# Optimization experiments

Hardware: AMD Instinct MI355X
Metric: run time of the kernel (lower is better)

Reference implementation:

```python
import jax, jax.numpy as jnp
import numpy as np

N_DIM = 256
NHIDDEN = 256
NLAYERS = 4
LAMDA = 0.5
ALPHA = 0.1
MODAL_WEIGHT = 1.0
N_SPEAKERS = 2
B_DIA = 100   # number of dialogues
L_DIA = 40    # utterances per dialogue
N_UTT = B_DIA * L_DIA


def _cos_sim_blocks(x, B, L):
    # per-dialogue cosine-similarity blocks: x [N, d] -> [B, L, L]
    xb = x.reshape(B, L, -1)
    xn = xb / jnp.linalg.norm(xb, axis=-1, keepdims=True)
    cos = jnp.einsum('bid,bjd->bij', xn, xn) * 0.99999
    return 1.0 - jnp.arccos(cos) / jnp.pi


def setup_inputs() -> dict:
    key = jax.random.key(0)
    ks = jax.random.split(key, 8)
    return {
        'a': jax.random.normal(ks[0], (N_UTT, N_DIM), jnp.float32),
        'v': jax.random.normal(ks[1], (N_UTT, N_DIM), jnp.float32),
        'l': jax.random.normal(ks[2], (N_UTT, N_DIM), jnp.float32),
        'qmask': jax.random.uniform(ks[3], (L_DIA, B_DIA, N_SPEAKERS), jnp.float32),
        'spk_emb': jax.random.normal(ks[4], (N_SPEAKERS, N_DIM), jnp.float32) * 0.02,
        'W0': jax.random.normal(ks[5], (N_DIM, NHIDDEN), jnp.float32) / np.sqrt(N_DIM).astype(np.float32),
        'b0': jnp.zeros((NHIDDEN,), jnp.float32),
        'Wconvs': jax.random.normal(ks[6], (NLAYERS, NHIDDEN, NHIDDEN), jnp.float32) / np.sqrt(NHIDDEN).astype(np.float32),
        'dia_len_each': L_DIA,
        'n_dialogues': B_DIA,
    }


def reference(a, v, l, qmask, spk_emb, W0, b0, Wconvs, dia_len_each, n_dialogues):
    B, L = n_dialogues, dia_len_each
    N = B * L
    M = 3  # modals 'avl'

    # --- speaker embedding added to text modality (use_speaker) ---
    # torch.cat([qmask[:x, i, :] for i, x in enumerate(dia_len)]) with equal lengths
    q = jnp.transpose(qmask, (1, 0, 2)).reshape(N, -1)   # [N, n_speakers]
    spk_idx = jnp.argmax(q, axis=-1)                      # [N]
    l = l + spk_emb[spk_idx]

    feats = [a, v, l]
    normed = [f / jnp.linalg.norm(f, axis=-1, keepdims=True) for f in feats]

    # --- create_big_adj: block-diag per-modal cosine-sim blocks + cross-modal diagonals ---
    adj = jnp.zeros((M * N, M * N), jnp.float32)
    idx = jnp.arange(N).reshape(B, L)
    rows = idx[:, :, None]   # [B, L, 1]
    cols = idx[:, None, :]   # [B, 1, L]
    ar = jnp.arange(N)
    for m in range(M):
        sim = _cos_sim_blocks(feats[m], B, L)            # [B, L, L]
        adj = adj.at[m * N + rows, m * N + cols].set(sim)
    for m in range(M):
        for n in range(M):
            if m == n:
                continue
            cs = jnp.sum(normed[m] * normed[n], axis=-1) * 0.99999
            dia_sim = 1.0 - jnp.arccos(cs) / jnp.pi
            adj = adj.at[m * N + ar, n * N + ar].set(dia_sim * MODAL_WEIGHT)
    d = jnp.sum(adj, axis=1)
    dinv = d ** -0.5
    adj = adj * dinv[:, None] * dinv[None, :]            # D^-1/2 A D^-1/2

    # --- GCNII_lyc propagation (eval mode, variant=False, no dropout) ---
    x = jnp.concatenate(feats, axis=0)                   # [3N, n_dim]
    h0 = jax.nn.relu(x @ W0 + b0)
    h = h0
    for i in range(NLAYERS):
        theta = float(np.log(LAMDA / (i + 1) + 1.0))
        hi = adj @ h
        support = (1.0 - ALPHA) * hi + ALPHA * h0
        h = jax.nn.relu(theta * (support @ Wconvs[i]) + (1.0 - theta) * support)
    feat = jnp.concatenate([x, h], axis=-1)              # use_residue

    # regroup modalities per utterance: [N, 3*(n_dim+nhidden)]
    out = jnp.concatenate([feat[:N], feat[N:2 * N], feat[2 * N:3 * N]], axis=-1)
    return out
```

## Files before the change

kernel.cpp:

```cpp
#include <hip/hip_runtime.h>
#include <hip/hip_bf16.h>

#define N_UTT 4000
#define NDIM 256
#define B_DIA 100
#define L_DIA 40
#define NLAYERS 4

typedef __attribute__((ext_vector_type(8))) short short8;
typedef __attribute__((ext_vector_type(4))) float f32x4;

union bfpk4 { __hip_bfloat16 h[4]; uint2 u; };

__global__ void k_wt(const float* __restrict__ W0, const float* __restrict__ Wc,
                     __hip_bfloat16* __restrict__ Wt) {
  int k0 = blockIdx.x * 64, n0 = blockIdx.y * 64, g = blockIdx.z;
  int t = threadIdx.x;
  const float* src = (g == 0) ? W0 : (Wc + (g - 1) * NDIM * NDIM);
  __shared__ float tile[64][65];
  #pragma unroll
  for (int it = 0; it < 16; it++) {
    int e = t + 256 * it;
    int row = e >> 6, col = e & 63;
    tile[row][col] = src[(k0 + row) * NDIM + n0 + col];
  }
  __syncthreads();
  #pragma unroll
  for (int it = 0; it < 16; it++) {
    int e = t + 256 * it;
    int row = e >> 6, col = e & 63;
    Wt[(g * NDIM + n0 + row) * NDIM + k0 + col] = __float2bfloat16(tile[col][row]);
  }
}

__global__ __launch_bounds__(512, 1) void k_main(
    const float* __restrict__ a, const float* __restrict__ v,
    const float* __restrict__ lf, const float* __restrict__ qmask,
    const float* __restrict__ spk, const float* __restrict__ b0,
    const __hip_bfloat16* __restrict__ Wt, float* __restrict__ out) {
  __shared__ __hip_bfloat16 xls[3][L_DIA][264];
  __shared__ __hip_bfloat16 hls[3][NDIM][L_DIA];
  __shared__ __hip_bfloat16 sext[3][L_DIA][136];
  __shared__ float invn[120];
  __shared__ float dinv[120];
  __shared__ float psum[120][4];

  int b = blockIdx.x;
  int t = threadIdx.x;
  int w = t >> 6, ln = t & 63;
  int l15 = ln & 15, lk = (ln >> 4) * 8;
  const float inv_pi = 0.31830988618379067f;

  {
    unsigned int* sz = (unsigned int*)&sext[0][0][0];
    #pragma unroll
    for (int e = t; e < 3 * L_DIA * 136 / 2; e += 512) sz[e] = 0u;
  }
  for (int e = t; e < 120 * 64; e += 512) {
    int r = e >> 6, c4 = e & 63;
    int m = r / L_DIA, p = r - m * L_DIA;
    int i = b * L_DIA + p;
    float4 val;
    if (m == 0)      val = ((const float4*)a)[i * 64 + c4];
    else if (m == 1) val = ((const float4*)v)[i * 64 + c4];
    else {
      val = ((const float4*)lf)[i * 64 + c4];
      float q0 = qmask[(p * B_DIA + b) * 2 + 0];
      float q1 = qmask[(p * B_DIA + b) * 2 + 1];
      int s = (q1 > q0) ? 1 : 0;
      float4 sv = ((const float4*)spk)[s * 64 + c4];
      val.x += sv.x; val.y += sv.y; val.z += sv.z; val.w += sv.w;
    }
    ((float4*)out)[i * 384 + m * 128 + c4] = val;
    bfpk4 pk;
    pk.h[0] = __float2bfloat16(val.x); pk.h[1] = __float2bfloat16(val.y);
    pk.h[2] = __float2bfloat16(val.z); pk.h[3] = __float2bfloat16(val.w);
    *(uint2*)&xls[m][p][c4 * 4] = pk.u;
  }
  __syncthreads();

  if (t < 480) {
    int r = t >> 2, q4 = t & 3;
    int m = r / L_DIA, p = r - m * L_DIA;
    float s = 0.f;
    #pragma unroll
    for (int j = 0; j < 64; j++) {
      float xv = __bfloat162float(xls[m][p][q4 * 64 + j]);
      s += xv * xv;
    }
    psum[r][q4] = s;
  }
  __syncthreads();
  if (t < 120) invn[t] = rsqrtf(psum[t][0] + psum[t][1] + psum[t][2] + psum[t][3]);
  __syncthreads();

  #pragma unroll
  for (int it = 0; it < 5; it++) {
    int tau = w + 8 * it;
    if (tau < 36) {
      int mA, mB, rt, ct, isdiag = 0, slotA = 0, slotB = 0;
      if (tau < 27) {
        mA = tau / 9; int rc = tau - mA * 9; rt = rc / 3; ct = rc - rt * 3; mB = mA;
      } else {
        int pi = (tau - 27) / 3; rt = (tau - 27) - pi * 3; ct = rt;
        mA = (pi == 2) ? 1 : 0; mB = (pi == 0) ? 1 : 2;
        slotA = (pi == 0) ? 40 : 80; slotB = (pi == 2) ? 80 : 40;
        isdiag = 1;
      }
      int arow = rt * 16 + l15; if (arow > 39) arow = 39;
      int bcol = ct * 16 + l15; if (bcol > 39) bcol = 39;
      f32x4 acc = {0.f, 0.f, 0.f, 0.f};
      #pragma unroll
      for (int k0 = 0; k0 < NDIM; k0 += 32) {
        short8 af = *(const short8*)&xls[mA][arow][k0 + lk];
        short8 bf = *(const short8*)&xls[mB][bcol][k0 + lk];
        acc = __builtin_amdgcn_mfma_f32_16x16x32_bf16(af, bf, acc, 0, 0, 0);
      }
      #pragma unroll
      for (int rr = 0; rr < 4; rr++) {
        int row = rt * 16 + (ln >> 4) * 4 + rr;
        int col = ct * 16 + l15;
        if (!isdiag) {
          if (row < 40 && col < 40) {
            float cs = acc[rr] * invn[mA * 40 + row] * invn[mA * 40 + col] * 0.99999f;
            cs = fminf(fmaxf(cs, -1.f), 1.f);
            sext[mA][row][col] = __float2bfloat16(1.f - acosf(cs) * inv_pi);
          }
        } else {
          if (l15 == ((ln >> 4) * 4 + rr) && row < 40) {
            float cs = acc[rr] * invn[mA * 40 + row] * invn[mB * 40 + row] * 0.99999f;
            cs = fminf(fmaxf(cs, -1.f), 1.f);
            __hip_bfloat16 vv = __float2bfloat16(1.f - acosf(cs) * inv_pi);
            sext[mA][row][slotA + row] = vv;
            sext[mB][row][slotB + row] = vv;
          }
        }
      }
    }
  }
  __syncthreads();

  if (t < 120) {
    int m = t / 40, p = t - m * 40;
    float d = 0.f;
    #pragma unroll 10
    for (int q = 0; q < 40; q++) d += __bfloat162float(sext[m][p][q]);
    d += __bfloat162float(sext[m][p][40 + p]) + __bfloat162float(sext[m][p][80 + p]);
    dinv[t] = rsqrtf(d);
  }
  __syncthreads();
  for (int e = t; e < 5040; e += 512) {
    if (e < 4800) {
      int m = e / 1600, rem = e - m * 1600;
      int p = rem / 40, q = rem - p * 40;
      sext[m][p][q] = __float2bfloat16(
          __bfloat162float(sext[m][p][q]) * 0.9f * dinv[m * 40 + p] * dinv[m * 40 + q]);
    } else {
      int idx = e - 4800;
      int m = idx / 80, j = idx - m * 80;
      int which = j / 40, p = j - which * 40;
      int pmx = which ? ((m == 2) ? 1 : 2) : ((m == 0) ? 1 : 0);
      int k = 40 * (1 + which) + p;
      sext[m][p][k] = __float2bfloat16(
          __bfloat162float(sext[m][p][k]) * 0.9f * dinv[m * 40 + p] * dinv[pmx * 40 + p]);
    }
  }
  __syncthreads();

  uint2 h0r[9][2];
  #pragma unroll
  for (int s = 0; s < 9; s++) {
    int m = s / 3, rt = s - m * 3;
    int arow = rt * 16 + l15; if (arow > 39) arow = 39;
    int p0 = rt * 16 + (ln >> 4) * 4;
    #pragma unroll
    for (int c = 0; c < 2; c++) {
      int col = w * 32 + c * 16 + l15;
      f32x4 acc = {0.f, 0.f, 0.f, 0.f};
      #pragma unroll
      for (int k0 = 0; k0 < NDIM; k0 += 32) {
        short8 af = *(const short8*)&xls[m][arow][k0 + lk];
        short8 bf = *(const short8*)&Wt[col * NDIM + k0 + lk];
        acc = __builtin_amdgcn_mfma_f32_16x16x32_bf16(af, bf, acc, 0, 0, 0);
      }
      float bias = b0[col];
      bfpk4 pk;
      #pragma unroll
      for (int rr = 0; rr < 4; rr++)
        pk.h[rr] = __float2bfloat16(fmaxf(acc[rr] + bias, 0.f));
      h0r[s][c] = pk.u;
      if (p0 < 40) *(uint2*)&hls[m][col][p0] = pk.u;
    }
  }
  __syncthreads();

  const float thetas[NLAYERS] = {0.40546510810816438f, 0.22314355131420976f,
                                 0.15415067982725836f, 0.11778303565638346f};
  #pragma unroll
  for (int li = 0; li < NLAYERS; li++) {
    float th = thetas[li], onemt = 1.f - th;
    const __hip_bfloat16* Wl = Wt + (li + 1) * NDIM * NDIM;
    f32x4 supreg[9][2];
    #pragma unroll
    for (int s = 0; s < 9; s++) {
      int m = s / 3, rt = s - m * 3;
      int pm0 = (m == 0) ? 1 : 0;
      int pm1 = (m == 2) ? 1 : 2;
      int arow = rt * 16 + l15; if (arow > 39) arow = 39;
      int p0 = rt * 16 + (ln >> 4) * 4;
      #pragma unroll
      for (int c = 0; c < 2; c++) {
        int col = w * 32 + c * 16 + l15;
        f32x4 acc = {0.f, 0.f, 0.f, 0.f};
        #pragma unroll
        for (int j = 0; j < 4; j++) {
          int kk = j * 32 + lk;
          int srcm, brow;
          if (kk < 40)       { srcm = m;   brow = kk; }
          else if (kk < 80)  { srcm = pm0; brow = kk - 40; }
          else if (kk < 120) { srcm = pm1; brow = kk - 80; }
          else               { srcm = m;   brow = 0; }
          short8 af = *(const short8*)&sext[m][arow][j * 32 + lk];
          short8 bf = *(const short8*)&hls[srcm][col][brow];
          acc = __builtin_amdgcn_mfma_f32_16x16x32_bf16(af, bf, acc, 0, 0, 0);
        }
        bfpk4 h0p; h0p.u = h0r[s][c];
        #pragma unroll
        for (int rr = 0; rr < 4; rr++)
          acc[rr] += 0.1f * __bfloat162float(h0p.h[rr]);
        supreg[s][c] = acc;
        if (p0 < 40) {
          #pragma unroll
          for (int rr = 0; rr < 4; rr++)
            xls[m][p0 + rr][col] = __float2bfloat16(acc[rr]);
        }
      }
    }
    __syncthreads();
    #pragma unroll
    for (int s = 0; s < 9; s++) {
      int m = s / 3, rt = s - m * 3;
      int arow = rt * 16 + l15; if (arow > 39) arow = 39;
      int p0 = rt * 16 + (ln >> 4) * 4;
      #pragma unroll
      for (int c = 0; c < 2; c++) {
        int col = w * 32 + c * 16 + l15;
        f32x4 acc = {0.f, 0.f, 0.f, 0.f};
        #pragma unroll
        for (int k0 = 0; k0 < NDIM; k0 += 32) {
          short8 af = *(const short8*)&xls[m][arow][k0 + lk];
          short8 bf = *(const short8*)&Wl[col * NDIM + k0 + lk];
          acc = __builtin_amdgcn_mfma_f32_16x16x32_bf16(af, bf, acc, 0, 0, 0);
        }
        if (p0 < 40) {
          if (li < NLAYERS - 1) {
            bfpk4 pk;
            #pragma unroll
            for (int rr = 0; rr < 4; rr++)
              pk.h[rr] = __float2bfloat16(
                  fmaxf(th * acc[rr] + onemt * supreg[s][c][rr], 0.f));
            *(uint2*)&hls[m][col][p0] = pk.u;
          } else {
            #pragma unroll
            for (int rr = 0; rr < 4; rr++)
              out[(b * L_DIA + p0 + rr) * 1536 + m * 512 + 256 + col] =
                  fmaxf(th * acc[rr] + onemt * supreg[s][c][rr], 0.f);
          }
        }
      }
    }
    __syncthreads();
  }
}

extern "C" void kernel_launch(void* const* d_in, const int* in_sizes, int n_in,
                              void* d_out, int out_size, void* d_ws, size_t ws_size,
                              hipStream_t stream) {
  const float* a     = (const float*)d_in[0];
  const float* v     = (const float*)d_in[1];
  const float* lf    = (const float*)d_in[2];
  const float* qmask = (const float*)d_in[3];
  const float* spk   = (const float*)d_in[4];
  const float* W0    = (const float*)d_in[5];
  const float* b0    = (const float*)d_in[6];
  const float* Wc    = (const float*)d_in[7];
  float* out = (float*)d_out;

  __hip_bfloat16* Wt = (__hip_bfloat16*)d_ws;

  k_wt<<<dim3(4, 4, 5), 256, 0, stream>>>(W0, Wc, Wt);
  k_main<<<B_DIA, 512, 0, stream>>>(a, v, lf, qmask, spk, b0, Wt, out);
}
```

Measured before the change: 78.05 us.

## Restructure MFMA loops for fragment reuse and drop fp32 support registers

Reorders the per-warp MFMA loops so the k-loop is outermost. Weight and h fragments are loaded once per k-step and reused across all nine row tiles, which removes repeated global and LDS fragment loads. The cosine-similarity stage is reassigned so three warps compute full per-modal blocks and three warps compute the cross-modal diagonals. The fp32 support accumulators held in registers are replaced by re-reading the bf16 support from LDS, which saves registers but rounds support to bf16 in the residual term. Bf16-to-float conversions are done with bit shifts, and the norm reduction uses vectorized LDS reads.

```diff
diff --git a/kernel.cpp b/kernel.cpp
--- a/kernel.cpp
+++ b/kernel.cpp
@@ -11,6 +11,12 @@
 typedef __attribute__((ext_vector_type(4))) float f32x4;
 
 union bfpk4 { __hip_bfloat16 h[4]; uint2 u; };
+
+static __device__ __forceinline__ float bf2f(__hip_bfloat16 h) {
+  union { float f; unsigned u; } x;
+  x.u = ((unsigned)*(unsigned short*)&h) << 16;
+  return x.f;
+}
 
 __global__ void k_wt(const float* __restrict__ W0, const float* __restrict__ Wc,
                      __hip_bfloat16* __restrict__ Wt) {
@@ -50,6 +56,15 @@
   int w = t >> 6, ln = t & 63;
   int l15 = ln & 15, lk = (ln >> 4) * 8;
   const float inv_pi = 0.31830988618379067f;
+
+  int arows[3], cols[2];
+  #pragma unroll
+  for (int rt = 0; rt < 3; rt++) {
+    int rr_ = rt * 16 + l15;
+    arows[rt] = (rr_ < L_DIA) ? rr_ : (L_DIA - 1);
+  }
+  #pragma unroll
+  for (int c = 0; c < 2; c++) cols[c] = w * 32 + c * 16 + l15;
 
   {
     unsigned int* sz = (unsigned int*)&sext[0][0][0];
@@ -84,9 +99,14 @@
     int m = r / L_DIA, p = r - m * L_DIA;
     float s = 0.f;
     #pragma unroll
-    for (int j = 0; j < 64; j++) {
-      float xv = __bfloat162float(xls[m][p][q4 * 64 + j]);
-      s += xv * xv;
+    for (int jj = 0; jj < 8; jj++) {
+      short8 vv = *(const short8*)&xls[m][p][q4 * 64 + jj * 8];
+      #pragma unroll
+      for (int e = 0; e < 8; e++) {
+        union { float f; unsigned u; } x;
+        x.u = ((unsigned)(unsigned short)vv[e]) << 16;
+        s += x.f * x.f;
+      }
     }
     psum[r][q4] = s;
   }
@@ -94,49 +114,71 @@
   if (t < 120) invn[t] = rsqrtf(psum[t][0] + psum[t][1] + psum[t][2] + psum[t][3]);
   __syncthreads();
 
-  #pragma unroll
-  for (int it = 0; it < 5; it++) {
-    int tau = w + 8 * it;
-    if (tau < 36) {
-      int mA, mB, rt, ct, isdiag = 0, slotA = 0, slotB = 0;
-      if (tau < 27) {
-        mA = tau / 9; int rc = tau - mA * 9; rt = rc / 3; ct = rc - rt * 3; mB = mA;
-      } else {
-        int pi = (tau - 27) / 3; rt = (tau - 27) - pi * 3; ct = rt;
-        mA = (pi == 2) ? 1 : 0; mB = (pi == 0) ? 1 : 2;
-        slotA = (pi == 0) ? 40 : 80; slotB = (pi == 2) ? 80 : 40;
-        isdiag = 1;
-      }
-      int arow = rt * 16 + l15; if (arow > 39) arow = 39;
-      int bcol = ct * 16 + l15; if (bcol > 39) bcol = 39;
-      f32x4 acc = {0.f, 0.f, 0.f, 0.f};
-      #pragma unroll
-      for (int k0 = 0; k0 < NDIM; k0 += 32) {
-        short8 af = *(const short8*)&xls[mA][arow][k0 + lk];
-        short8 bf = *(const short8*)&xls[mB][bcol][k0 + lk];
-        acc = __builtin_amdgcn_mfma_f32_16x16x32_bf16(af, bf, acc, 0, 0, 0);
-      }
-      #pragma unroll
-      for (int rr = 0; rr < 4; rr++) {
-        int row = rt * 16 + (ln >> 4) * 4 + rr;
-        int col = ct * 16 + l15;
-        if (!isdiag) {
-          if (row < 40 && col < 40) {
-            float cs = acc[rr] * invn[mA * 40 + row] * invn[mA * 40 + col] * 0.99999f;
+  if (w < 3) {
+    int mA = w;
+    f32x4 sacc[3][3];
+    #pragma unroll
+    for (int rt = 0; rt < 3; rt++)
+      #pragma unroll
+      for (int ct = 0; ct < 3; ct++) sacc[rt][ct] = (f32x4){0.f,0.f,0.f,0.f};
+    #pragma unroll
+    for (int k0 = 0; k0 < NDIM; k0 += 32) {
+      short8 fr[3];
+      #pragma unroll
+      for (int rt = 0; rt < 3; rt++)
+        fr[rt] = *(const short8*)&xls[mA][arows[rt]][k0 + lk];
+      #pragma unroll
+      for (int rt = 0; rt < 3; rt++)
+        #pragma unroll
+        for (int ct = 0; ct < 3; ct++)
+          sacc[rt][ct] = __builtin_amdgcn_mfma_f32_16x16x32_bf16(fr[rt], fr[ct], sacc[rt][ct], 0, 0, 0);
+    }
+    #pragma unroll
+    for (int rt = 0; rt < 3; rt++)
+      #pragma unroll
+      for (int ct = 0; ct < 3; ct++)
+        #pragma unroll
+        for (int rr = 0; rr < 4; rr++) {
+          int row = rt * 16 + (ln >> 4) * 4 + rr;
+          int col = ct * 16 + l15;
+          if (row < L_DIA && col < L_DIA) {
+            float cs = sacc[rt][ct][rr] * invn[mA * 40 + row] * invn[mA * 40 + col] * 0.99999f;
             cs = fminf(fmaxf(cs, -1.f), 1.f);
             sext[mA][row][col] = __float2bfloat16(1.f - acosf(cs) * inv_pi);
           }
-        } else {
-          if (l15 == ((ln >> 4) * 4 + rr) && row < 40) {
-            float cs = acc[rr] * invn[mA * 40 + row] * invn[mB * 40 + row] * 0.99999f;
-            cs = fminf(fmaxf(cs, -1.f), 1.f);
-            __hip_bfloat16 vv = __float2bfloat16(1.f - acosf(cs) * inv_pi);
-            sext[mA][row][slotA + row] = vv;
-            sext[mB][row][slotB + row] = vv;
-          }
-        }
-      }
-    }
+        }
+  } else if (w < 6) {
+    int pi = w - 3;
+    int mA = (pi == 2) ? 1 : 0, mB = (pi == 0) ? 1 : 2;
+    int slotA = (pi == 0) ? 40 : 80, slotB = (pi == 2) ? 80 : 40;
+    f32x4 dacc[3];
+    #pragma unroll
+    for (int rt = 0; rt < 3; rt++) dacc[rt] = (f32x4){0.f,0.f,0.f,0.f};
+    #pragma unroll
+    for (int k0 = 0; k0 < NDIM; k0 += 32) {
+      short8 frA[3], frB[3];
+      #pragma unroll
+      for (int rt = 0; rt < 3; rt++) {
+        frA[rt] = *(const short8*)&xls[mA][arows[rt]][k0 + lk];
+        frB[rt] = *(const short8*)&xls[mB][arows[rt]][k0 + lk];
+      }
+      #pragma unroll
+      for (int rt = 0; rt < 3; rt++)
+        dacc[rt] = __builtin_amdgcn_mfma_f32_16x16x32_bf16(frA[rt], frB[rt], dacc[rt], 0, 0, 0);
+    }
+    #pragma unroll
+    for (int rt = 0; rt < 3; rt++)
+      #pragma unroll
+      for (int rr = 0; rr < 4; rr++) {
+        int row = rt * 16 + (ln >> 4) * 4 + rr;
+        if (l15 == ((ln >> 4) * 4 + rr) && row < L_DIA) {
+          float cs = dacc[rt][rr] * invn[mA * 40 + row] * invn[mB * 40 + row] * 0.99999f;
+          cs = fminf(fmaxf(cs, -1.f), 1.f);
+          __hip_bfloat16 vv = __float2bfloat16(1.f - acosf(cs) * inv_pi);
+          sext[mA][row][slotA + row] = vv;
+          sext[mB][row][slotB + row] = vv;
+        }
+      }
   }
   __syncthreads();
 
@@ -144,8 +186,8 @@
     int m = t / 40, p = t - m * 40;
     float d = 0.f;
     #pragma unroll 10
-    for (int q = 0; q < 40; q++) d += __bfloat162float(sext[m][p][q]);
-    d += __bfloat162float(sext[m][p][40 + p]) + __bfloat162float(sext[m][p][80 + p]);
+    for (int q = 0; q < 40; q++) d += bf2f(sext[m][p][q]);
+    d += bf2f(sext[m][p][40 + p]) + bf2f(sext[m][p][80 + p]);
     dinv[t] = rsqrtf(d);
   }
   __syncthreads();
@@ -154,7 +196,7 @@
       int m = e / 1600, rem = e - m * 1600;
       int p = rem / 40, q = rem - p * 40;
       sext[m][p][q] = __float2bfloat16(
-          __bfloat162float(sext[m][p][q]) * 0.9f * dinv[m * 40 + p] * dinv[m * 40 + q]);
+          bf2f(sext[m][p][q]) * 0.9f * dinv[m * 40 + p] * dinv[m * 40 + q]);
     } else {
       int idx = e - 4800;
       int m = idx / 80, j = idx - m * 80;
@@ -162,34 +204,47 @@
       int pmx = which ? ((m == 2) ? 1 : 2) : ((m == 0) ? 1 : 0);
       int k = 40 * (1 + which) + p;
       sext[m][p][k] = __float2bfloat16(
-          __bfloat162float(sext[m][p][k]) * 0.9f * dinv[m * 40 + p] * dinv[pmx * 40 + p]);
+          bf2f(sext[m][p][k]) * 0.9f * dinv[m * 40 + p] * dinv[pmx * 40 + p]);
     }
   }
   __syncthreads();
 
   uint2 h0r[9][2];
-  #pragma unroll
-  for (int s = 0; s < 9; s++) {
-    int m = s / 3, rt = s - m * 3;
-    int arow = rt * 16 + l15; if (arow > 39) arow = 39;
-    int p0 = rt * 16 + (ln >> 4) * 4;
-    #pragma unroll
-    for (int c = 0; c < 2; c++) {
-      int col = w * 32 + c * 16 + l15;
-      f32x4 acc = {0.f, 0.f, 0.f, 0.f};
-      #pragma unroll
-      for (int k0 = 0; k0 < NDIM; k0 += 32) {
-        short8 af = *(const short8*)&xls[m][arow][k0 + lk];
-        short8 bf = *(const short8*)&Wt[col * NDIM + k0 + lk];
-        acc = __builtin_amdgcn_mfma_f32_16x16x32_bf16(af, bf, acc, 0, 0, 0);
-      }
-      float bias = b0[col];
-      bfpk4 pk;
-      #pragma unroll
-      for (int rr = 0; rr < 4; rr++)
-        pk.h[rr] = __float2bfloat16(fmaxf(acc[rr] + bias, 0.f));
-      h0r[s][c] = pk.u;
-      if (p0 < 40) *(uint2*)&hls[m][col][p0] = pk.u;
+  {
+    f32x4 acc[9][2];
+    #pragma unroll
+    for (int s = 0; s < 9; s++)
+      #pragma unroll
+      for (int c = 0; c < 2; c++) acc[s][c] = (f32x4){0.f,0.f,0.f,0.f};
+    #pragma unroll
+    for (int k0 = 0; k0 < NDIM; k0 += 32) {
+      short8 bfw[2];
+      #pragma unroll
+      for (int c = 0; c < 2; c++)
+        bfw[c] = *(const short8*)&Wt[cols[c] * NDIM + k0 + lk];
+      short8 af[9];
+      #pragma unroll
+      for (int s = 0; s < 9; s++)
+        af[s] = *(const short8*)&xls[s / 3][arows[s % 3]][k0 + lk];
+      #pragma unroll
+      for (int s = 0; s < 9; s++)
+        #pragma unroll
+        for (int c = 0; c < 2; c++)
+          acc[s][c] = __builtin_amdgcn_mfma_f32_16x16x32_bf16(af[s], bfw[c], acc[s][c], 0, 0, 0);
+    }
+    #pragma unroll
+    for (int s = 0; s < 9; s++) {
+      int p0 = (s % 3) * 16 + (ln >> 4) * 4;
+      #pragma unroll
+      for (int c = 0; c < 2; c++) {
+        float bias = b0[cols[c]];
+        bfpk4 pk;
+        #pragma unroll
+        for (int rr = 0; rr < 4; rr++)
+          pk.h[rr] = __float2bfloat16(fmaxf(acc[s][c][rr] + bias, 0.f));
+        h0r[s][c] = pk.u;
+        if (p0 < L_DIA) *(uint2*)&hls[s / 3][cols[c]][p0] = pk.u;
+      }
     }
   }
   __syncthreads();
@@ -200,71 +255,101 @@
   for (int li = 0; li < NLAYERS; li++) {
     float th = thetas[li], onemt = 1.f - th;
     const __hip_bfloat16* Wl = Wt + (li + 1) * NDIM * NDIM;
-    f32x4 supreg[9][2];
-    #pragma unroll
-    for (int s = 0; s < 9; s++) {
-      int m = s / 3, rt = s - m * 3;
-      int pm0 = (m == 0) ? 1 : 0;
-      int pm1 = (m == 2) ? 1 : 2;
-      int arow = rt * 16 + l15; if (arow > 39) arow = 39;
-      int p0 = rt * 16 + (ln >> 4) * 4;
-      #pragma unroll
-      for (int c = 0; c < 2; c++) {
-        int col = w * 32 + c * 16 + l15;
-        f32x4 acc = {0.f, 0.f, 0.f, 0.f};
-        #pragma unroll
-        for (int j = 0; j < 4; j++) {
+
+    {
+      f32x4 acc[9][2];
+      #pragma unroll
+      for (int s = 0; s < 9; s++)
+        #pragma unroll
+        for (int c = 0; c < 2; c++) acc[s][c] = (f32x4){0.f,0.f,0.f,0.f};
+      #pragma unroll
+      for (int j = 0; j < 4; j++) {
+        short8 bfv[3][2];
+        #pragma unroll
+        for (int mm = 0; mm < 3; mm++) {
+          int pm0 = (mm == 0) ? 1 : 0, pm1 = (mm == 2) ? 1 : 2;
           int kk = j * 32 + lk;
           int srcm, brow;
-          if (kk < 40)       { srcm = m;   brow = kk; }
+          if (kk < 40)       { srcm = mm;  brow = kk; }
           else if (kk < 80)  { srcm = pm0; brow = kk - 40; }
           else if (kk < 120) { srcm = pm1; brow = kk - 80; }
-          else               { srcm = m;   brow = 0; }
-          short8 af = *(const short8*)&sext[m][arow][j * 32 + lk];
-          short8 bf = *(const short8*)&hls[srcm][col][brow];
-          acc = __builtin_amdgcn_mfma_f32_16x16x32_bf16(af, bf, acc, 0, 0, 0);
-        }
-        bfpk4 h0p; h0p.u = h0r[s][c];
-        #pragma unroll
-        for (int rr = 0; rr < 4; rr++)
-          acc[rr] += 0.1f * __bfloat162float(h0p.h[rr]);
-        supreg[s][c] = acc;
-        if (p0 < 40) {
+          else               { srcm = pm1; brow = 32; }
           #pragma unroll
-          for (int rr = 0; rr < 4; rr++)
-            xls[m][p0 + rr][col] = __float2bfloat16(acc[rr]);
+          for (int c = 0; c < 2; c++)
+            bfv[mm][c] = *(const short8*)&hls[srcm][cols[c]][brow];
+        }
+        short8 af[9];
+        #pragma unroll
+        for (int s = 0; s < 9; s++)
+          af[s] = *(const short8*)&sext[s / 3][arows[s % 3]][j * 32 + lk];
+        #pragma unroll
+        for (int s = 0; s < 9; s++)
+          #pragma unroll
+          for (int c = 0; c < 2; c++)
+            acc[s][c] = __builtin_amdgcn_mfma_f32_16x16x32_bf16(af[s], bfv[s / 3][c], acc[s][c], 0, 0, 0);
+      }
+      #pragma unroll
+      for (int s = 0; s < 9; s++) {
+        int p0 = (s % 3) * 16 + (ln >> 4) * 4;
+        #pragma unroll
+        for (int c = 0; c < 2; c++) {
+          bfpk4 h0p; h0p.u = h0r[s][c];
+          if (p0 < L_DIA) {
+            #pragma unroll
+            for (int rr = 0; rr < 4; rr++)
+              xls[s / 3][p0 + rr][cols[c]] =
+                  __float2bfloat16(acc[s][c][rr] + 0.1f * bf2f(h0p.h[rr]));
+          }
         }
       }
     }
     __syncthreads();
-    #pragma unroll
-    for (int s = 0; s < 9; s++) {
-      int m = s / 3, rt = s - m * 3;
-      int arow = rt * 16 + l15; if (arow > 39) arow = 39;
-      int p0 = rt * 16 + (ln >> 4) * 4;
-      #pragma unroll
-      for (int c = 0; c < 2; c++) {
-        int col = w * 32 + c * 16 + l15;
-        f32x4 acc = {0.f, 0.f, 0.f, 0.f};
-        #pragma unroll
-        for (int k0 = 0; k0 < NDIM; k0 += 32) {
-          short8 af = *(const short8*)&xls[m][arow][k0 + lk];
-          short8 bf = *(const short8*)&Wl[col * NDIM + k0 + lk];
-          acc = __builtin_amdgcn_mfma_f32_16x16x32_bf16(af, bf, acc, 0, 0, 0);
-        }
-        if (p0 < 40) {
+
+    {
+      f32x4 o[9][2];
+      #pragma unroll
+      for (int s = 0; s < 9; s++)
+        #pragma unroll
+        for (int c = 0; c < 2; c++) o[s][c] = (f32x4){0.f,0.f,0.f,0.f};
+      #pragma unroll
+      for (int k0 = 0; k0 < NDIM; k0 += 32) {
+        short8 bfw[2];
+        #pragma unroll
+        for (int c = 0; c < 2; c++)
+          bfw[c] = *(const short8*)&Wl[cols[c] * NDIM + k0 + lk];
+        short8 af[9];
+        #pragma unroll
+        for (int s = 0; s < 9; s++)
+          af[s] = *(const short8*)&xls[s / 3][arows[s % 3]][k0 + lk];
+        #pragma unroll
+        for (int s = 0; s < 9; s++)
+          #pragma unroll
+          for (int c = 0; c < 2; c++)
+            o[s][c] = __builtin_amdgcn_mfma_f32_16x16x32_bf16(af[s], bfw[c], o[s][c], 0, 0, 0);
+      }
+      #pragma unroll
+      for (int s = 0; s < 9; s++) {
+        int m = s / 3;
+        int p0 = (s % 3) * 16 + (ln >> 4) * 4;
+        if (p0 >= L_DIA) continue;
+        #pragma unroll
+        for (int c = 0; c < 2; c++) {
+          int col = cols[c];
           if (li < NLAYERS - 1) {
             bfpk4 pk;
             #pragma unroll
-            for (int rr = 0; rr < 4; rr++)
-              pk.h[rr] = __float2bfloat16(
-                  fmaxf(th * acc[rr] + onemt * supreg[s][c][rr], 0.f));
+            for (int rr = 0; rr < 4; rr++) {
+              float supv = bf2f(xls[m][p0 + rr][col]);
+              pk.h[rr] = __float2bfloat16(fmaxf(th * o[s][c][rr] + onemt * supv, 0.f));
+            }
             *(uint2*)&hls[m][col][p0] = pk.u;
           } else {
             #pragma unroll
-            for (int rr = 0; rr < 4; rr++)
+            for (int rr = 0; rr < 4; rr++) {
+              float supv = bf2f(xls[m][p0 + rr][col]);
               out[(b * L_DIA + p0 + rr) * 1536 + m * 512 + 256 + col] =
-                  fmaxf(th * acc[rr] + onemt * supreg[s][c][rr], 0.f);
+                  fmaxf(th * o[s][c][rr] + onemt * supv, 0.f);
+            }
           }
         }
       }
```

New measurement: 63.63 us. -18.5%, faster.
